# Kernel optimization log

Measured on AMD Instinct MI355X. Metric: run time of the kernel, lower is better.

## Reference

```python
import jax, jax.numpy as jnp
import numpy as np

N = 262144
E = 2097152
IMG = 120.0
VOX = 16.0
GRID = 8  # ceil(120/16)
NUM_GRIDS = GRID * GRID
EPS = 1e-5


def setup_inputs() -> dict:
    key = jax.random.key(0)
    ks = jax.random.split(key, 16)
    x = jax.random.normal(ks[0], (N, 1), dtype=jnp.float32)
    pos = jax.random.uniform(ks[1], (N, 3), dtype=jnp.float32) * IMG
    edge_index = jax.random.randint(ks[2], (2, E), 0, N, dtype=jnp.int64)
    # conv1: PointNetConv-style local linear on concat([x_j, pos_j - pos_i]) -> 16
    W1 = jax.random.normal(ks[3], (1 + 3, 16), dtype=jnp.float32) * 0.3
    b1 = jax.random.normal(ks[4], (16,), dtype=jnp.float32) * 0.05
    bn1_mean = jax.random.uniform(ks[5], (16,), dtype=jnp.float32)
    bn1_var = jax.random.uniform(ks[6], (16,), dtype=jnp.float32)
    bn1_w = jax.random.uniform(ks[7], (16,), dtype=jnp.float32)
    bn1_b = jax.random.uniform(ks[8], (16,), dtype=jnp.float32)
    # conv2: 16 -> 32
    W2 = jax.random.normal(ks[9], (16 + 3, 32), dtype=jnp.float32) * 0.2
    b2 = jax.random.normal(ks[10], (32,), dtype=jnp.float32) * 0.05
    bn2_mean = jax.random.uniform(ks[11], (32,), dtype=jnp.float32)
    bn2_var = jax.random.uniform(ks[12], (32,), dtype=jnp.float32)
    bn2_w = jax.random.uniform(ks[13], (32,), dtype=jnp.float32)
    bn2_b = jax.random.uniform(ks[14], (32,), dtype=jnp.float32)
    return dict(x=x, pos=pos, edge_index=edge_index,
                W1=W1, b1=b1, bn1_mean=bn1_mean, bn1_var=bn1_var, bn1_w=bn1_w, bn1_b=bn1_b,
                W2=W2, b2=b2, bn2_mean=bn2_mean, bn2_var=bn2_var, bn2_w=bn2_w, bn2_b=bn2_b)


def _conv_bn_relu(x, pos, src, dst, W, b, mean, var, gamma, beta):
    # message: linear(concat([x_j, pos_j - pos_i])), max aggregation over incoming edges
    rel = pos[src] - pos[dst]                       # [E, 3]
    msg = jnp.concatenate([x[src], rel], axis=1) @ W + b  # [E, C_out]
    agg = jax.ops.segment_max(msg, dst, num_segments=N)   # [N, C_out]
    agg = jnp.where(jnp.isneginf(agg), 0.0, agg)    # nodes with no incoming edges -> 0
    # BatchNorm1d in eval mode (running stats) + ReLU
    y = (agg - mean) * jax.lax.rsqrt(var + EPS) * gamma + beta
    return jax.nn.relu(y)


def reference(x, pos, edge_index, W1, b1, bn1_mean, bn1_var, bn1_w, bn1_b,
              W2, b2, bn2_mean, bn2_var, bn2_w, bn2_b):
    src, dst = edge_index[0], edge_index[1]
    h1 = _conv_bn_relu(x, pos, src, dst, W1, b1, bn1_mean, bn1_var, bn1_w, bn1_b)
    h2 = _conv_bn_relu(h1, pos, src, dst, W2, b2, bn2_mean, bn2_var, bn2_w, bn2_b)
    # MaxPoolingX: voxel-grid cluster on pos[:, :2] with voxel size 16 over 120x120 -> 8x8 grid
    gx = jnp.floor(pos[:, 0] / VOX).astype(jnp.int32)
    gy = jnp.floor(pos[:, 1] / VOX).astype(jnp.int32)
    cluster = jnp.clip(gx + gy * GRID, 0, NUM_GRIDS - 1)
    pooled = jax.ops.segment_max(h2, cluster, num_segments=NUM_GRIDS)  # [64, 32]
    pooled = jnp.where(jnp.isneginf(pooled), 0.0, pooled)
    return pooled
```

## Files before the change

### kernel.cpp

```cpp
#include <hip/hip_runtime.h>
#include <hip/hip_fp16.h>

#define N_NODES 262144
#define N_EDGES 2097152
#define EPS_BN 1e-5f
#define NBUCK 1024
#define BCAP 2560

__device__ __forceinline__ unsigned enc(float f) {
    unsigned u = __float_as_uint(f);
    return (u & 0x80000000u) ? ~u : (u | 0x80000000u);
}
__device__ __forceinline__ float dec(unsigned u) {
    unsigned b = (u & 0x80000000u) ? (u & 0x7FFFFFFFu) : ~u;
    return __uint_as_float(b);
}

__global__ __launch_bounds__(256) void part_k(const int* __restrict__ ei,
                                              int* __restrict__ bcur,
                                              unsigned* __restrict__ pairs2) {
    __shared__ int hh[NBUCK], bb[NBUCK];
    int t = threadIdx.x;
    for (int i = t; i < NBUCK; i += 256) hh[i] = 0;
    __syncthreads();
    int base = blockIdx.x * 4096;
    for (int k = 0; k < 16; ++k) {
        int d = ei[N_EDGES + base + k * 256 + t];
        atomicAdd(&hh[d >> 8], 1);
    }
    __syncthreads();
    for (int i = t; i < NBUCK; i += 256) {
        int c = hh[i];
        bb[i] = c ? atomicAdd(&bcur[i], c) : 0;
        hh[i] = 0;
    }
    __syncthreads();
    for (int k = 0; k < 16; ++k) {
        int e = base + k * 256 + t;
        int d = ei[N_EDGES + e], s = ei[e];
        int b = d >> 8;
        int r = atomicAdd(&hh[b], 1);
        int slot = bb[b] + r;
        if (slot < BCAP)
            pairs2[(size_t)b * BCAP + slot] = (unsigned)s | ((unsigned)(d & 255) << 18);
    }
}

__global__ __launch_bounds__(256) void alpha_k(const float* __restrict__ x,
                                               const float* __restrict__ pos,
                                               const float* __restrict__ W1,
                                               const float* __restrict__ b1,
                                               float* __restrict__ alpha) {
    int t = blockIdx.x * 256 + threadIdx.x;
    int n = t >> 4, ch = t & 15;
    float a = b1[ch] + W1[ch] * x[n]
            + W1[16 + ch] * pos[3*n] + W1[32 + ch] * pos[3*n+1] + W1[48 + ch] * pos[3*n+2];
    alpha[t] = a;
}

__global__ __launch_bounds__(256) void conv1_push(
    const float* __restrict__ alpha, const float* __restrict__ pos,
    const unsigned* __restrict__ pairs2, const int* __restrict__ bcur,
    const float* __restrict__ W1,
    const float* __restrict__ mean, const float* __restrict__ var,
    const float* __restrict__ gamma, const float* __restrict__ beta_bn,
    const float* __restrict__ W2, const float* __restrict__ b2,
    __half* __restrict__ beta)
{
    __shared__ unsigned agg[256 * 16];
    for (int i = threadIdx.x; i < 256 * 16; i += 256) agg[i] = 0u;
    int b = blockIdx.x;
    int cnt = min(bcur[b], BCAP);
    const unsigned* P = pairs2 + (size_t)b * BCAP;
    int g = threadIdx.x >> 4, ch = threadIdx.x & 15;
    __syncthreads();

    int e = g;
    for (; e + 48 < cnt; e += 64) {
        unsigned p0 = P[e], p1 = P[e+16], p2 = P[e+32], p3 = P[e+48];
        float a0 = alpha[(p0 & 0x3FFFFu) * 16 + ch];
        float a1 = alpha[(p1 & 0x3FFFFu) * 16 + ch];
        float a2 = alpha[(p2 & 0x3FFFFu) * 16 + ch];
        float a3 = alpha[(p3 & 0x3FFFFu) * 16 + ch];
        atomicMax(&agg[(p0 >> 18) * 16 + ch], enc(a0));
        atomicMax(&agg[(p1 >> 18) * 16 + ch], enc(a1));
        atomicMax(&agg[(p2 >> 18) * 16 + ch], enc(a2));
        atomicMax(&agg[(p3 >> 18) * 16 + ch], enc(a3));
    }
    for (; e < cnt; e += 16) {
        unsigned p = P[e];
        float a = alpha[(p & 0x3FFFFu) * 16 + ch];
        atomicMax(&agg[(p >> 18) * 16 + ch], enc(a));
    }
    __syncthreads();

    int k = threadIdx.x & 15;
    float w1x = W1[16 + k], w1y = W1[32 + k], w1z = W1[48 + k];
    float sc1 = gamma[k] * rsqrtf(var[k] + EPS_BN);
    float sh1 = beta_bn[k] - mean[k] * sc1;
    int dbase = b * 256;
    for (int slot = threadIdx.x; slot < 4096; slot += 256) {
        int d = slot >> 4, n = dbase + d;
        unsigned u = agg[slot];
        float px = pos[3*n], py = pos[3*n+1], pz = pos[3*n+2];
        float v = u ? (dec(u) - (w1x*px + w1y*py + w1z*pz)) : 0.0f;
        ((float*)agg)[slot] = fmaxf(v * sc1 + sh1, 0.0f);
    }
    __syncthreads();

    int c = threadIdx.x & 31, row = threadIdx.x >> 5;
    float wc[16];
#pragma unroll
    for (int q = 0; q < 16; ++q) wc[q] = W2[q * 32 + c];
    float wxc = W2[512 + c], wyc = W2[544 + c], wzc = W2[576 + c], bc = b2[c];
    for (int d = row; d < 256; d += 8) {
        const float* h = (const float*)agg + d * 16;
        float bv = bc;
#pragma unroll
        for (int q = 0; q < 16; ++q) bv += wc[q] * h[q];
        int n = dbase + d;
        bv += wxc * pos[3*n] + wyc * pos[3*n+1] + wzc * pos[3*n+2];
        beta[(size_t)n * 32 + c] = __float2half(bv);
    }
}

__global__ __launch_bounds__(256) void conv2_push(
    const __half* __restrict__ beta, const float* __restrict__ pos,
    const unsigned* __restrict__ pairs2, const int* __restrict__ bcur,
    const float* __restrict__ W2,
    const float* __restrict__ mean, const float* __restrict__ var,
    const float* __restrict__ gamma, const float* __restrict__ beta_bn,
    unsigned* __restrict__ pool)
{
    __shared__ unsigned agg[256 * 32];
    __shared__ unsigned lpool[2048];
    for (int i = threadIdx.x; i < 256 * 32; i += 256) agg[i] = 0u;
    for (int i = threadIdx.x; i < 2048; i += 256) lpool[i] = 0u;
    int b = blockIdx.x;
    int cnt = min(bcur[b], BCAP);
    const unsigned* P = pairs2 + (size_t)b * BCAP;
    int g = threadIdx.x >> 5, ch = threadIdx.x & 31;
    float wrx = W2[512 + ch], wry = W2[544 + ch], wrz = W2[576 + ch];
    float sc = gamma[ch] * rsqrtf(var[ch] + EPS_BN);
    float sh = beta_bn[ch] - mean[ch] * sc;
    __syncthreads();

    int e = g;
    for (; e + 24 < cnt; e += 32) {
        unsigned p0 = P[e], p1 = P[e+8], p2 = P[e+16], p3 = P[e+24];
        float a0 = __half2float(beta[(size_t)(p0 & 0x3FFFFu) * 32 + ch]);
        float a1 = __half2float(beta[(size_t)(p1 & 0x3FFFFu) * 32 + ch]);
        float a2 = __half2float(beta[(size_t)(p2 & 0x3FFFFu) * 32 + ch]);
        float a3 = __half2float(beta[(size_t)(p3 & 0x3FFFFu) * 32 + ch]);
        atomicMax(&agg[(p0 >> 18) * 32 + ch], enc(a0));
        atomicMax(&agg[(p1 >> 18) * 32 + ch], enc(a1));
        atomicMax(&agg[(p2 >> 18) * 32 + ch], enc(a2));
        atomicMax(&agg[(p3 >> 18) * 32 + ch], enc(a3));
    }
    for (; e < cnt; e += 8) {
        unsigned p = P[e];
        float a = __half2float(beta[(size_t)(p & 0x3FFFFu) * 32 + ch]);
        atomicMax(&agg[(p >> 18) * 32 + ch], enc(a));
    }
    __syncthreads();

    int dbase = b * 256;
    for (int slot = threadIdx.x; slot < 8192; slot += 256) {
        int d = slot >> 5, n = dbase + d;
        unsigned u = agg[slot];
        float px = pos[3*n], py = pos[3*n+1], pz = pos[3*n+2];
        float v = u ? (dec(u) - (wrx*px + wry*py + wrz*pz)) : 0.0f;
        float y = fmaxf(v * sc + sh, 0.0f);
        int gx = (int)floorf(px * (1.0f/16.0f));
        int gy = (int)floorf(py * (1.0f/16.0f));
        int cl = min(max(gx + gy * 8, 0), 63);
        atomicMax(&lpool[cl * 32 + ch], enc(y));
    }
    __syncthreads();
    for (int i = threadIdx.x; i < 2048; i += 256) {
        unsigned u = lpool[i];
        if (u > pool[i]) atomicMax(&pool[i], u);
    }
}

__global__ __launch_bounds__(256) void pool_decode(const unsigned* __restrict__ pool,
                                                   float* __restrict__ out) {
    int i = blockIdx.x * 256 + threadIdx.x;
    unsigned u = pool[i];
    out[i] = (u == 0u) ? 0.0f : dec(u);
}

extern "C" void kernel_launch(void* const* d_in, const int* in_sizes, int n_in,
                              void* d_out, int out_size, void* d_ws, size_t ws_size,
                              hipStream_t stream) {
    const float* x    = (const float*)d_in[0];
    const float* pos  = (const float*)d_in[1];
    const int*   ei   = (const int*)d_in[2];
    const float* W1   = (const float*)d_in[3];
    const float* b1   = (const float*)d_in[4];
    const float* bn1m = (const float*)d_in[5];
    const float* bn1v = (const float*)d_in[6];
    const float* bn1w = (const float*)d_in[7];
    const float* bn1b = (const float*)d_in[8];
    const float* W2   = (const float*)d_in[9];
    const float* b2   = (const float*)d_in[10];
    const float* bn2m = (const float*)d_in[11];
    const float* bn2v = (const float*)d_in[12];
    const float* bn2w = (const float*)d_in[13];
    const float* bn2b = (const float*)d_in[14];

    size_t N = N_NODES;
    unsigned* pool   = (unsigned*)d_ws;
    int* bcur        = (int*)(pool + 2048);
    unsigned* pairs2 = (unsigned*)(bcur + 1024);
    float* alpha     = (float*)(pairs2 + (size_t)NBUCK * BCAP);
    __half* beta     = (__half*)(alpha + 16 * N);

    hipMemsetAsync(d_ws, 0, (size_t)(2048 + 1024) * 4, stream);

    part_k      <<<N_EDGES/4096, 256, 0, stream>>>(ei, bcur, pairs2);
    alpha_k     <<<N_NODES*16/256, 256, 0, stream>>>(x, pos, W1, b1, alpha);
    conv1_push  <<<NBUCK, 256, 0, stream>>>(alpha, pos, pairs2, bcur,
                                            W1, bn1m, bn1v, bn1w, bn1b, W2, b2, beta);
    conv2_push  <<<NBUCK, 256, 0, stream>>>(beta, pos, pairs2, bcur,
                                            W2, bn2m, bn2v, bn2w, bn2b, pool);
    pool_decode <<<8, 256, 0, stream>>>(pool, (float*)d_out);
}
```

Measured before the change: 276.9 us.

## Halve destination bucket size to 128 nodes and deepen gather unroll to eight

Destinations are now bucketed 128 nodes per bucket instead of 256, which doubles the bucket count to 2048 and the number of blocks in the two conv kernels while halving their shared-memory aggregation tiles. The partition kernel handles 8192 edges per block so it launches fewer blocks. Inside the conv kernels the gather loop now issues eight independent loads before the atomic maxima instead of four, and launch bounds set occupancy hints. The goal is better occupancy and more memory-level parallelism on the random gathers. The cost is extra register pressure, and each bucket's capacity (1280 against a mean of 1024 edges) leaves less headroom for overflow, where edges past capacity are silently dropped.

```diff
diff --git a/kernel.cpp b/kernel.cpp
--- a/kernel.cpp
+++ b/kernel.cpp
@@ -4,8 +4,8 @@
 #define N_NODES 262144
 #define N_EDGES 2097152
 #define EPS_BN 1e-5f
-#define NBUCK 1024
-#define BCAP 2560
+#define NBUCK 2048
+#define BCAP 1280
 
 __device__ __forceinline__ unsigned enc(float f) {
     unsigned u = __float_as_uint(f);
@@ -23,10 +23,10 @@
     int t = threadIdx.x;
     for (int i = t; i < NBUCK; i += 256) hh[i] = 0;
     __syncthreads();
-    int base = blockIdx.x * 4096;
-    for (int k = 0; k < 16; ++k) {
+    int base = blockIdx.x * 8192;
+    for (int k = 0; k < 32; ++k) {
         int d = ei[N_EDGES + base + k * 256 + t];
-        atomicAdd(&hh[d >> 8], 1);
+        atomicAdd(&hh[d >> 7], 1);
     }
     __syncthreads();
     for (int i = t; i < NBUCK; i += 256) {
@@ -35,14 +35,14 @@
         hh[i] = 0;
     }
     __syncthreads();
-    for (int k = 0; k < 16; ++k) {
+    for (int k = 0; k < 32; ++k) {
         int e = base + k * 256 + t;
         int d = ei[N_EDGES + e], s = ei[e];
-        int b = d >> 8;
+        int b = d >> 7;
         int r = atomicAdd(&hh[b], 1);
         int slot = bb[b] + r;
         if (slot < BCAP)
-            pairs2[(size_t)b * BCAP + slot] = (unsigned)s | ((unsigned)(d & 255) << 18);
+            pairs2[(size_t)b * BCAP + slot] = (unsigned)s | ((unsigned)(d & 127) << 18);
     }
 }
 
@@ -58,7 +58,7 @@
     alpha[t] = a;
 }
 
-__global__ __launch_bounds__(256) void conv1_push(
+__global__ __launch_bounds__(256, 8) void conv1_push(
     const float* __restrict__ alpha, const float* __restrict__ pos,
     const unsigned* __restrict__ pairs2, const int* __restrict__ bcur,
     const float* __restrict__ W1,
@@ -67,8 +67,8 @@
     const float* __restrict__ W2, const float* __restrict__ b2,
     __half* __restrict__ beta)
 {
-    __shared__ unsigned agg[256 * 16];
-    for (int i = threadIdx.x; i < 256 * 16; i += 256) agg[i] = 0u;
+    __shared__ unsigned agg[128 * 16];
+    for (int i = threadIdx.x; i < 128 * 16; i += 256) agg[i] = 0u;
     int b = blockIdx.x;
     int cnt = min(bcur[b], BCAP);
     const unsigned* P = pairs2 + (size_t)b * BCAP;
@@ -76,16 +76,16 @@
     __syncthreads();
 
     int e = g;
-    for (; e + 48 < cnt; e += 64) {
-        unsigned p0 = P[e], p1 = P[e+16], p2 = P[e+32], p3 = P[e+48];
-        float a0 = alpha[(p0 & 0x3FFFFu) * 16 + ch];
-        float a1 = alpha[(p1 & 0x3FFFFu) * 16 + ch];
-        float a2 = alpha[(p2 & 0x3FFFFu) * 16 + ch];
-        float a3 = alpha[(p3 & 0x3FFFFu) * 16 + ch];
-        atomicMax(&agg[(p0 >> 18) * 16 + ch], enc(a0));
-        atomicMax(&agg[(p1 >> 18) * 16 + ch], enc(a1));
-        atomicMax(&agg[(p2 >> 18) * 16 + ch], enc(a2));
-        atomicMax(&agg[(p3 >> 18) * 16 + ch], enc(a3));
+    for (; e + 112 < cnt; e += 128) {
+        unsigned p[8];
+        float a[8];
+#pragma unroll
+        for (int q = 0; q < 8; ++q) p[q] = P[e + q * 16];
+#pragma unroll
+        for (int q = 0; q < 8; ++q) a[q] = alpha[(p[q] & 0x3FFFFu) * 16 + ch];
+#pragma unroll
+        for (int q = 0; q < 8; ++q)
+            atomicMax(&agg[(p[q] >> 18) * 16 + ch], enc(a[q]));
     }
     for (; e < cnt; e += 16) {
         unsigned p = P[e];
@@ -98,8 +98,8 @@
     float w1x = W1[16 + k], w1y = W1[32 + k], w1z = W1[48 + k];
     float sc1 = gamma[k] * rsqrtf(var[k] + EPS_BN);
     float sh1 = beta_bn[k] - mean[k] * sc1;
-    int dbase = b * 256;
-    for (int slot = threadIdx.x; slot < 4096; slot += 256) {
+    int dbase = b * 128;
+    for (int slot = threadIdx.x; slot < 2048; slot += 256) {
         int d = slot >> 4, n = dbase + d;
         unsigned u = agg[slot];
         float px = pos[3*n], py = pos[3*n+1], pz = pos[3*n+2];
@@ -113,7 +113,7 @@
 #pragma unroll
     for (int q = 0; q < 16; ++q) wc[q] = W2[q * 32 + c];
     float wxc = W2[512 + c], wyc = W2[544 + c], wzc = W2[576 + c], bc = b2[c];
-    for (int d = row; d < 256; d += 8) {
+    for (int d = row; d < 128; d += 8) {
         const float* h = (const float*)agg + d * 16;
         float bv = bc;
 #pragma unroll
@@ -124,7 +124,7 @@
     }
 }
 
-__global__ __launch_bounds__(256) void conv2_push(
+__global__ __launch_bounds__(256, 6) void conv2_push(
     const __half* __restrict__ beta, const float* __restrict__ pos,
     const unsigned* __restrict__ pairs2, const int* __restrict__ bcur,
     const float* __restrict__ W2,
@@ -132,9 +132,9 @@
     const float* __restrict__ gamma, const float* __restrict__ beta_bn,
     unsigned* __restrict__ pool)
 {
-    __shared__ unsigned agg[256 * 32];
+    __shared__ unsigned agg[128 * 32];
     __shared__ unsigned lpool[2048];
-    for (int i = threadIdx.x; i < 256 * 32; i += 256) agg[i] = 0u;
+    for (int i = threadIdx.x; i < 128 * 32; i += 256) agg[i] = 0u;
     for (int i = threadIdx.x; i < 2048; i += 256) lpool[i] = 0u;
     int b = blockIdx.x;
     int cnt = min(bcur[b], BCAP);
@@ -146,16 +146,17 @@
     __syncthreads();
 
     int e = g;
-    for (; e + 24 < cnt; e += 32) {
-        unsigned p0 = P[e], p1 = P[e+8], p2 = P[e+16], p3 = P[e+24];
-        float a0 = __half2float(beta[(size_t)(p0 & 0x3FFFFu) * 32 + ch]);
-        float a1 = __half2float(beta[(size_t)(p1 & 0x3FFFFu) * 32 + ch]);
-        float a2 = __half2float(beta[(size_t)(p2 & 0x3FFFFu) * 32 + ch]);
-        float a3 = __half2float(beta[(size_t)(p3 & 0x3FFFFu) * 32 + ch]);
-        atomicMax(&agg[(p0 >> 18) * 32 + ch], enc(a0));
-        atomicMax(&agg[(p1 >> 18) * 32 + ch], enc(a1));
-        atomicMax(&agg[(p2 >> 18) * 32 + ch], enc(a2));
-        atomicMax(&agg[(p3 >> 18) * 32 + ch], enc(a3));
+    for (; e + 56 < cnt; e += 64) {
+        unsigned p[8];
+        float a[8];
+#pragma unroll
+        for (int q = 0; q < 8; ++q) p[q] = P[e + q * 8];
+#pragma unroll
+        for (int q = 0; q < 8; ++q)
+            a[q] = __half2float(beta[(size_t)(p[q] & 0x3FFFFu) * 32 + ch]);
+#pragma unroll
+        for (int q = 0; q < 8; ++q)
+            atomicMax(&agg[(p[q] >> 18) * 32 + ch], enc(a[q]));
     }
     for (; e < cnt; e += 8) {
         unsigned p = P[e];
@@ -164,8 +165,8 @@
     }
     __syncthreads();
 
-    int dbase = b * 256;
-    for (int slot = threadIdx.x; slot < 8192; slot += 256) {
+    int dbase = b * 128;
+    for (int slot = threadIdx.x; slot < 4096; slot += 256) {
         int d = slot >> 5, n = dbase + d;
         unsigned u = agg[slot];
         float px = pos[3*n], py = pos[3*n+1], pz = pos[3*n+2];
@@ -212,13 +213,13 @@
     size_t N = N_NODES;
     unsigned* pool   = (unsigned*)d_ws;
     int* bcur        = (int*)(pool + 2048);
-    unsigned* pairs2 = (unsigned*)(bcur + 1024);
+    unsigned* pairs2 = (unsigned*)(bcur + NBUCK);
     float* alpha     = (float*)(pairs2 + (size_t)NBUCK * BCAP);
     __half* beta     = (__half*)(alpha + 16 * N);
 
-    hipMemsetAsync(d_ws, 0, (size_t)(2048 + 1024) * 4, stream);
-
-    part_k      <<<N_EDGES/4096, 256, 0, stream>>>(ei, bcur, pairs2);
+    hipMemsetAsync(d_ws, 0, (size_t)(2048 + NBUCK) * 4, stream);
+
+    part_k      <<<N_EDGES/8192, 256, 0, stream>>>(ei, bcur, pairs2);
     alpha_k     <<<N_NODES*16/256, 256, 0, stream>>>(x, pos, W1, b1, alpha);
     conv1_push  <<<NBUCK, 256, 0, stream>>>(alpha, pos, pairs2, bcur,
                                             W1, bn1m, bn1v, bn1w, bn1b, W2, b2, beta);
```

Result: slower. 322.9 us (+16.6%).
